# Optimization experiments

Measured on AMD Instinct MI355X. Metric: run time of the kernel, lower is better.

The kernel has to match this reference:

```python
import jax, jax.numpy as jnp
import numpy as np

N_NODES = 50000
N_EDGES = 800000
D_IN = 16


def gcn_conv(x, edge_index, W, b, n_nodes):
    """PyG GCNConv: x' = D^{-1/2} (A + I) D^{-1/2} X W + b (add_self_loops=True)."""
    h = x @ W  # [N, d_out] - transform before propagate (small d => cheaper)
    src = jnp.concatenate([edge_index[0], jnp.arange(n_nodes)])  # add self-loops
    dst = jnp.concatenate([edge_index[1], jnp.arange(n_nodes)])
    deg = jax.ops.segment_sum(jnp.ones_like(dst, dtype=h.dtype), dst,
                              num_segments=n_nodes)  # in-degree incl. self-loop
    deg_inv_sqrt = jnp.where(deg > 0, jax.lax.rsqrt(deg), 0.0)
    norm = deg_inv_sqrt[src] * deg_inv_sqrt[dst]  # [E+N]
    msg = h[src] * norm[:, None]                  # gather + scale
    out = jax.ops.segment_sum(msg, dst, num_segments=n_nodes)  # scatter-add
    return out + b


def setup_inputs() -> dict:
    key = jax.random.key(0)
    ks = jax.random.split(key, 16)
    d = D_IN
    x = jax.random.normal(ks[0], (N_NODES, d), dtype=jnp.float32)
    edge_index = jax.random.randint(ks[1], (2, N_EDGES), 0, N_NODES, dtype=jnp.int64)

    def glorot(k, fan_in, fan_out):
        s = (6.0 / (fan_in + fan_out)) ** 0.5
        return jax.random.uniform(k, (fan_in, fan_out), jnp.float32, -s, s)

    return {
        "x": x,
        "edge_index": edge_index,
        "W1": glorot(ks[2], d, 2 * d),      "b1": jnp.zeros((2 * d,), jnp.float32),
        "W2": glorot(ks[3], 2 * d, 4 * d),  "b2": jnp.zeros((4 * d,), jnp.float32),
        "W3": glorot(ks[4], 4 * d, 8 * d),  "b3": jnp.zeros((8 * d,), jnp.float32),
        "Wl1": glorot(ks[5], 8 * d, 4 * d), "bl1": jnp.zeros((4 * d,), jnp.float32),
        "Wl2": glorot(ks[6], 4 * d, 2 * d), "bl2": jnp.zeros((2 * d,), jnp.float32),
        "Wl3": glorot(ks[7], 2 * d, d),     "bl3": jnp.zeros((d,), jnp.float32),
    }


def reference(x, edge_index, W1, b1, W2, b2, W3, b3, Wl1, bl1, Wl2, bl2, Wl3, bl3):
    n = x.shape[0]
    # note: original applies relu twice per conv; relu is idempotent
    out = jax.nn.relu(gcn_conv(x, edge_index, W1, b1, n))
    out = jax.nn.relu(gcn_conv(out, edge_index, W2, b2, n))
    out = jax.nn.relu(gcn_conv(out, edge_index, W3, b3, n))
    out = jax.nn.relu(out @ Wl1 + bl1)
    out = jax.nn.relu(out @ Wl2 + bl2)
    out = jax.nn.relu(out @ Wl3 + bl3)
    return out
```

## Files before the change

### kernel.cpp

```cpp
#include <hip/hip_runtime.h>

#define TPB 256
#define TE  2048
#define MAXB 6144

typedef _Float16 half_t;
typedef _Float16 half4 __attribute__((ext_vector_type(4)));
typedef _Float16 half8 __attribute__((ext_vector_type(8)));
typedef float float8v __attribute__((ext_vector_type(8)));

static inline int cdiv(int a, int b) { return (a + b - 1) / b; }


__global__ void k_zero_int(int* p, int n) {
    int i = blockIdx.x * blockDim.x + threadIdx.x;
    if (i < n) p[i] = 0;
}

__global__ void k_bhist(const int* __restrict__ dst, int* __restrict__ gcnt,
                        int e, int nb) {
    __shared__ int lc[256];
    for (int t = threadIdx.x; t < nb; t += TPB) lc[t] = 0;
    __syncthreads();
    for (int i = blockIdx.x * TPB + threadIdx.x; i < e; i += gridDim.x * TPB)
        atomicAdd(&lc[dst[i] >> 8], 1);
    __syncthreads();
    for (int t = threadIdx.x; t < nb; t += TPB) {
        int v = lc[t];
        if (v) atomicAdd(&gcnt[t], v);
    }
}

__global__ void __launch_bounds__(TPB)
k_binscatter(const int* __restrict__ src, const int* __restrict__ dst,
             const int* __restrict__ gcnt, int* __restrict__ bcur2,
             unsigned int* __restrict__ gbuf, int e, int nb) {
    __shared__ int lcnt[256], loffs[256], lcur[256], gres[256];
    __shared__ int ss[256];
    __shared__ unsigned int ldata[TE];
    const int tid = threadIdx.x;
    const int base = blockIdx.x * TE;
    const int cnt = min(TE, e - base);

    {
        int v = (tid < nb) ? gcnt[tid] : 0;
        ss[tid] = v;
        __syncthreads();
        for (int d = 1; d < 256; d <<= 1) {
            int x2 = (tid >= d) ? ss[tid - d] : 0;
            __syncthreads();
            ss[tid] += x2;
            __syncthreads();
        }
        gres[tid] = ss[tid] - v;
        lcnt[tid] = 0;
    }
    __syncthreads();

    unsigned int myv[TE / TPB];
    int myb[TE / TPB];
#pragma unroll
    for (int k = 0; k < TE / TPB; ++k) {
        int j = tid + k * TPB;
        if (j < cnt) {
            int d = dst[base + j], s = src[base + j];
            int b = d >> 8;
            myv[k] = ((unsigned)b << 24) | ((unsigned)(d & 255) << 16) | (unsigned)s;
            myb[k] = b;
            atomicAdd(&lcnt[b], 1);
        } else myb[k] = -1;
    }
    __syncthreads();
    {
        int v = (tid < nb) ? lcnt[tid] : 0;
        ss[tid] = v;
        __syncthreads();
        for (int d = 1; d < 256; d <<= 1) {
            int x2 = (tid >= d) ? ss[tid - d] : 0;
            __syncthreads();
            ss[tid] += x2;
            __syncthreads();
        }
        if (tid < nb) { loffs[tid] = ss[tid] - v; lcur[tid] = ss[tid] - v; }
    }
    __syncthreads();
    if (tid < nb && lcnt[tid]) gres[tid] += atomicAdd(&bcur2[tid], lcnt[tid]);
#pragma unroll
    for (int k = 0; k < TE / TPB; ++k) {
        if (myb[k] >= 0) {
            int p = atomicAdd(&lcur[myb[k]], 1);
            ldata[p] = myv[k];
        }
    }
    __syncthreads();
    for (int j = tid; j < cnt; j += TPB) {
        unsigned int v = ldata[j];
        int b = v >> 24;
        gbuf[gres[b] + (j - loffs[b])] = v & 0xFFFFFFu;
    }
}

__global__ void __launch_bounds__(TPB)
k_csr(const unsigned int* __restrict__ gbuf, const int* __restrict__ gcnt,
      const float* __restrict__ x, int* __restrict__ offs,
      float* __restrict__ dinv, unsigned short* __restrict__ ssrc,
      half_t* __restrict__ G, int n, int e, int nb) {
    __shared__ int ss[256], cnt[256], loffs2[256], lcur2[256];
    __shared__ float sdinv[256];
    __shared__ unsigned short stage[MAXB];
    const int b = blockIdx.x;
    const int t = threadIdx.x;

    {
        int v = (t < nb) ? gcnt[t] : 0;
        ss[t] = v;
        __syncthreads();
        for (int d = 1; d < 256; d <<= 1) {
            int x2 = (t >= d) ? ss[t - d] : 0;
            __syncthreads();
            ss[t] += x2;
            __syncthreads();
        }
    }
    const int s0 = (b > 0) ? ss[b - 1] : 0;
    const int s1 = ss[b];
    const int m = s1 - s0;
    __syncthreads();
    cnt[t] = 0;
    __syncthreads();
    for (int j = t; j < m; j += TPB)
        atomicAdd(&cnt[(gbuf[s0 + j] >> 16) & 255], 1);
    __syncthreads();
    {
        int v = cnt[t];
        ss[t] = v;
        __syncthreads();
        for (int d = 1; d < 256; d <<= 1) {
            int x2 = (t >= d) ? ss[t - d] : 0;
            __syncthreads();
            ss[t] += x2;
            __syncthreads();
        }
        loffs2[t] = ss[t] - v;
        lcur2[t] = ss[t] - v;
        float di = rsqrtf((float)v + 1.0f);
        sdinv[t] = di;
        int node = b * 256 + t;
        if (node < n) {
            offs[node] = s0 + loffs2[t];
            dinv[node] = di;
        }
    }
    __syncthreads();
    for (int j = t; j < m; j += TPB) {
        unsigned int v = gbuf[s0 + j];
        int p = atomicAdd(&lcur2[(v >> 16) & 255], 1);
        stage[p] = (unsigned short)(v & 0xFFFFu);
    }
    __syncthreads();
    for (int j = t; j < m; j += TPB) ssrc[s0 + j] = stage[j];
    if (b == 0 && t == 0) offs[n] = e;

    const int base = b * 256;
    const int cn = min(256, n - base);
    const float4* X4 = (const float4*)x;
    half4* G4 = (half4*)G;
    for (int j = t; j < cn * 4; j += TPB) {
        int nl = j >> 2, k4 = j & 3;
        float4 v = X4[(size_t)(base + nl) * 4 + k4];
        float d = sdinv[nl];
        half4 h;
        h.x = (half_t)(v.x * d); h.y = (half_t)(v.y * d);
        h.z = (half_t)(v.z * d); h.w = (half_t)(v.w * d);
        G4[(size_t)(base + nl) * 4 + k4] = h;
    }
}

template<int DI, int DO, int R, bool SCALE, bool OUT_HALF, bool WHALF>
__global__ void __launch_bounds__(TPB, 4)
k_conv(const int* __restrict__ offs, const unsigned short* __restrict__ ssrc,
       const half_t* __restrict__ G, const float* __restrict__ dinv,
       const float* __restrict__ W, const float* __restrict__ b,
       void* __restrict__ outp, int n) {
    constexpr int CT = DO / 4;
    constexpr int RT = TPB / CT;
    constexpr int TM = RT * R;
    constexpr int K4 = DI / 4;
    constexpr int PX = K4 + 1;
    constexpr int C  = DI / 8;
    static_assert(TM * C == TPB, "gather/gemm tile mismatch");
    __shared__ float4 sW4[WHALF ? 1 : DI * CT];
    __shared__ half4  sWh[WHALF ? DI * CT : 1];
    __shared__ float4 sX4[TM * PX];
    __shared__ int soffs[TM + 1];
    __shared__ unsigned char perm[TM];
    const int tid = threadIdx.x;
    const int r0 = blockIdx.x * TM;

    const float4* Wg = (const float4*)W;
    for (int t = tid; t < DI * CT; t += TPB) {
        float4 w = Wg[t];
        if (WHALF) {
            half4 h;
            h.x = (half_t)w.x; h.y = (half_t)w.y;
            h.z = (half_t)w.z; h.w = (half_t)w.w;
            sWh[t] = h;
        } else {
            sW4[t] = w;
        }
    }
    if (tid <= TM) soffs[tid] = offs[min(r0 + tid, n)];
    __syncthreads();
    if (tid < TM) {
        int d = soffs[tid + 1] - soffs[tid];
        int rank = 0;
        for (int j = 0; j < TM; ++j) {
            int dj = soffs[j + 1] - soffs[j];
            rank += (dj > d) || (dj == d && j < tid);
        }
        perm[rank] = (unsigned char)tid;
    }
    __syncthreads();

    {
        int slot = tid / C;
        int gc = tid - slot * C;
        int lrow = perm[slot];
        int row = r0 + lrow;
        float8v acc;
#pragma unroll
        for (int q = 0; q < 8; ++q) acc[q] = 0.f;
        if (row < n) {
            const half8* Grow = (const half8*)G;
            half8 hs = Grow[(size_t)row * C + gc];
#pragma unroll
            for (int q = 0; q < 8; ++q) acc[q] = (float)hs[q];
            int s0 = soffs[lrow], s1 = soffs[lrow + 1];
            int j = s0;
            for (; j + 3 < s1; j += 4) {
                int sa = ssrc[j], sb = ssrc[j + 1];
                int sc = ssrc[j + 2], sd = ssrc[j + 3];
                half8 ga = Grow[(size_t)sa * C + gc];
                half8 gb = Grow[(size_t)sb * C + gc];
                half8 gch = Grow[(size_t)sc * C + gc];
                half8 gd = Grow[(size_t)sd * C + gc];
#pragma unroll
                for (int q = 0; q < 8; ++q)
                    acc[q] += ((float)ga[q] + (float)gb[q]) + ((float)gch[q] + (float)gd[q]);
            }
            for (; j < s1; ++j) {
                half8 ga = Grow[(size_t)ssrc[j] * C + gc];
#pragma unroll
                for (int q = 0; q < 8; ++q) acc[q] += (float)ga[q];
            }
            float di = dinv[row];
#pragma unroll
            for (int q = 0; q < 8; ++q) acc[q] *= di;
        }
        sX4[lrow * PX + 2 * gc]     = make_float4(acc[0], acc[1], acc[2], acc[3]);
        sX4[lrow * PX + 2 * gc + 1] = make_float4(acc[4], acc[5], acc[6], acc[7]);
    }
    __syncthreads();

    const int c = tid & (CT - 1);
    const int rg = tid / CT;
    const int rbase = rg * R;
    float4 acc[R];
#pragma unroll
    for (int r = 0; r < R; ++r) acc[r] = make_float4(0.f, 0.f, 0.f, 0.f);

#pragma unroll 2
    for (int k4 = 0; k4 < K4; ++k4) {
        float4 xv[R];
#pragma unroll
        for (int r = 0; r < R; ++r) xv[r] = sX4[(rbase + r) * PX + k4];
#pragma unroll
        for (int kk = 0; kk < 4; ++kk) {
            float4 wv;
            if (WHALF) {
                half4 wh = sWh[(k4 * 4 + kk) * CT + c];
                wv = make_float4((float)wh.x, (float)wh.y, (float)wh.z, (float)wh.w);
            } else {
                wv = sW4[(k4 * 4 + kk) * CT + c];
            }
#pragma unroll
            for (int r = 0; r < R; ++r) {
                float xs = (kk == 0) ? xv[r].x : (kk == 1) ? xv[r].y
                         : (kk == 2) ? xv[r].z : xv[r].w;
                acc[r].x += xs * wv.x; acc[r].y += xs * wv.y;
                acc[r].z += xs * wv.z; acc[r].w += xs * wv.w;
            }
        }
    }

    float4 bc = ((const float4*)b)[c];
#pragma unroll
    for (int r = 0; r < R; ++r) {
        int row = r0 + rbase + r;
        if (row < n) {
            float4 o;
            o.x = fmaxf(acc[r].x + bc.x, 0.f);
            o.y = fmaxf(acc[r].y + bc.y, 0.f);
            o.z = fmaxf(acc[r].z + bc.z, 0.f);
            o.w = fmaxf(acc[r].w + bc.w, 0.f);
            if (SCALE) {
                float d = dinv[row];
                o.x *= d; o.y *= d; o.z *= d; o.w *= d;
            }
            if (OUT_HALF) {
                half4 h;
                h.x = (half_t)o.x; h.y = (half_t)o.y;
                h.z = (half_t)o.z; h.w = (half_t)o.w;
                ((half4*)outp)[(size_t)row * CT + c] = h;
            } else {
                ((float4*)outp)[(size_t)row * CT + c] = o;
            }
        }
    }
}

__global__ void __launch_bounds__(256, 2)
k_head(const half_t* __restrict__ X,
       const float* __restrict__ W1, const float* __restrict__ b1,
       const float* __restrict__ W2, const float* __restrict__ b2,
       const float* __restrict__ W3, const float* __restrict__ b3,
       float* __restrict__ out, int n) {
    __shared__ half_t hW1[128 * 64];
    __shared__ half_t hW2[64 * 32];
    __shared__ half_t hW3[32 * 16];
    __shared__ float h1[64 * 65];
    __shared__ float h2[64 * 33];
    const int tid = threadIdx.x;
    const int r0 = blockIdx.x * 64;

    for (int t = tid; t < 128 * 64; t += 256) hW1[t] = (half_t)W1[t];
    for (int t = tid; t < 64 * 32; t += 256) hW2[t] = (half_t)W2[t];
    for (int t = tid; t < 32 * 16; t += 256) hW3[t] = (half_t)W3[t];
    __syncthreads();

    {
        const int c4 = tid & 15;
        const int rowg = tid >> 4;
        const half8* Xr = (const half8*)X;
        float acc[4][4];
#pragma unroll
        for (int r = 0; r < 4; ++r)
#pragma unroll
            for (int j = 0; j < 4; ++j) acc[r][j] = 0.f;
        for (int k8 = 0; k8 < 16; ++k8) {
            half8 xh[4];
#pragma unroll
            for (int r = 0; r < 4; ++r) {
                int row = r0 + rowg * 4 + r;
                if (row < n) xh[r] = Xr[(size_t)row * 16 + k8];
                else { half8 z; for (int q = 0; q < 8; ++q) z[q] = (half_t)0.f; xh[r] = z; }
            }
#pragma unroll
            for (int q = 0; q < 8; ++q) {
                int k = k8 * 8 + q;
                half4 w = *(const half4*)&hW1[k * 64 + c4 * 4];
                float w0 = (float)w.x, w1 = (float)w.y, w2 = (float)w.z, w3 = (float)w.w;
#pragma unroll
                for (int r = 0; r < 4; ++r) {
                    float xs = (float)xh[r][q];
                    acc[r][0] += xs * w0; acc[r][1] += xs * w1;
                    acc[r][2] += xs * w2; acc[r][3] += xs * w3;
                }
            }
        }
        float4 bc = ((const float4*)b1)[c4];
#pragma unroll
        for (int r = 0; r < 4; ++r) {
            int rl = rowg * 4 + r;
            h1[rl * 65 + c4 * 4 + 0] = fmaxf(acc[r][0] + bc.x, 0.f);
            h1[rl * 65 + c4 * 4 + 1] = fmaxf(acc[r][1] + bc.y, 0.f);
            h1[rl * 65 + c4 * 4 + 2] = fmaxf(acc[r][2] + bc.z, 0.f);
            h1[rl * 65 + c4 * 4 + 3] = fmaxf(acc[r][3] + bc.w, 0.f);
        }
    }
    __syncthreads();

    {
        const int c4 = tid & 7;
        const int rowg = tid >> 3;
        float acc[2][4];
#pragma unroll
        for (int r = 0; r < 2; ++r)
#pragma unroll
            for (int j = 0; j < 4; ++j) acc[r][j] = 0.f;
#pragma unroll 4
        for (int k = 0; k < 64; ++k) {
            half4 w = *(const half4*)&hW2[k * 32 + c4 * 4];
            float w0 = (float)w.x, w1 = (float)w.y, w2 = (float)w.z, w3 = (float)w.w;
#pragma unroll
            for (int r = 0; r < 2; ++r) {
                float xs = h1[(rowg * 2 + r) * 65 + k];
                acc[r][0] += xs * w0; acc[r][1] += xs * w1;
                acc[r][2] += xs * w2; acc[r][3] += xs * w3;
            }
        }
        float4 bc = ((const float4*)b2)[c4];
#pragma unroll
        for (int r = 0; r < 2; ++r) {
            int rl = rowg * 2 + r;
            h2[rl * 33 + c4 * 4 + 0] = fmaxf(acc[r][0] + bc.x, 0.f);
            h2[rl * 33 + c4 * 4 + 1] = fmaxf(acc[r][1] + bc.y, 0.f);
            h2[rl * 33 + c4 * 4 + 2] = fmaxf(acc[r][2] + bc.z, 0.f);
            h2[rl * 33 + c4 * 4 + 3] = fmaxf(acc[r][3] + bc.w, 0.f);
        }
    }
    __syncthreads();

    {
        const int c4 = tid & 3;
        const int rl = tid >> 2;
        float a0 = 0.f, a1 = 0.f, a2 = 0.f, a3 = 0.f;
#pragma unroll 4
        for (int k = 0; k < 32; ++k) {
            half4 w = *(const half4*)&hW3[k * 16 + c4 * 4];
            float xs = h2[rl * 33 + k];
            a0 += xs * (float)w.x; a1 += xs * (float)w.y;
            a2 += xs * (float)w.z; a3 += xs * (float)w.w;
        }
        int row = r0 + rl;
        if (row < n) {
            float4 bc = ((const float4*)b3)[c4];
            float4 o;
            o.x = fmaxf(a0 + bc.x, 0.f);
            o.y = fmaxf(a1 + bc.y, 0.f);
            o.z = fmaxf(a2 + bc.z, 0.f);
            o.w = fmaxf(a3 + bc.w, 0.f);
            ((float4*)out)[(size_t)row * 4 + c4] = o;
        }
    }
}

extern "C" void kernel_launch(void* const* d_in, const int* in_sizes, int n_in,
                              void* d_out, int out_size, void* d_ws, size_t ws_size,
                              hipStream_t stream) {
    const float* x   = (const float*)d_in[0];
    const int*   ei  = (const int*)d_in[1];
    const float* W1  = (const float*)d_in[2];
    const float* bb1 = (const float*)d_in[3];
    const float* W2  = (const float*)d_in[4];
    const float* bb2 = (const float*)d_in[5];
    const float* W3  = (const float*)d_in[6];
    const float* bb3 = (const float*)d_in[7];
    const float* Wl1 = (const float*)d_in[8];
    const float* bl1 = (const float*)d_in[9];
    const float* Wl2 = (const float*)d_in[10];
    const float* bl2 = (const float*)d_in[11];
    const float* Wl3 = (const float*)d_in[12];
    const float* bl3 = (const float*)d_in[13];
    float* out = (float*)d_out;

    const int n = in_sizes[0] / 16;
    const int e = in_sizes[1] / 2;
    const int* src = ei;
    const int* dst = ei + e;
    const int nb = cdiv(n, 256);

    char* p = (char*)d_ws;
    auto alloc = [&](size_t bytes) {
        char* r = p;
        p += (bytes + 255) & ~(size_t)255;
        return r;
    };
    float*          dinv   = (float*)         alloc((size_t)n * 4);
    int*            offs   = (int*)           alloc((size_t)(n + 1) * 4);
    int*            gcnt   = (int*)           alloc(256 * 4);
    int*            bcur2  = (int*)           alloc(256 * 4);
    unsigned int*   gbuf   = (unsigned int*)  alloc((size_t)e * 4);
    unsigned short* ssrc   = (unsigned short*)alloc((size_t)e * 2);
    half_t*         H1     = (half_t*)        alloc((size_t)n * 64 * 2);
    half_t*         H2     = (half_t*)        alloc((size_t)n * 32 * 2);
    half_t*         X3h    = (half_t*)        alloc((size_t)n * 128 * 2);

    k_zero_int<<<2, 256, 0, stream>>>(gcnt, 512);
    k_bhist<<<512, TPB, 0, stream>>>(dst, gcnt, e, nb);
    k_binscatter<<<cdiv(e, TE), TPB, 0, stream>>>(src, dst, gcnt, bcur2, gbuf, e, nb);
    k_csr<<<nb, TPB, 0, stream>>>(gbuf, gcnt, x, offs, dinv, ssrc, H1, n, e, nb);

    k_conv<16, 32, 4, true, true, false><<<cdiv(n, 128), TPB, 0, stream>>>(
        offs, ssrc, H1, dinv, W1, bb1, H2, n);
    k_conv<32, 64, 4, true, true, false><<<cdiv(n, 64), TPB, 0, stream>>>(
        offs, ssrc, H2, dinv, W2, bb2, H1, n);
    k_conv<64, 128, 4, false, true, true><<<cdiv(n, 32), TPB, 0, stream>>>(
        offs, ssrc, H1, dinv, W3, bb3, X3h, n);

    k_head<<<cdiv(n, 64), 256, 0, stream>>>(X3h, Wl1, bl1, Wl2, bl2, Wl3, bl3, out, n);
}
```

Before: 222.0 us.

## Use packed fp16 dot2 instructions for conv and head GEMMs, drop degree sort

Replaces the fp32 FMA inner products in the conv GEMM (when FDOT is set) and in the first head layer with v_dot2 fp16 instructions. Weights are repacked into a k-contiguous half8 layout and gathered activations are staged in shared memory as fp16. It also removes the per-block degree-ranking permutation used to balance gather work across threads. This cuts ALU work and shared-memory footprint, at the cost of lower precision in the activations and possible gather load imbalance.

```diff
diff --git a/kernel.cpp b/kernel.cpp
--- a/kernel.cpp
+++ b/kernel.cpp
@@ -5,11 +5,27 @@
 #define MAXB 6144
 
 typedef _Float16 half_t;
+typedef _Float16 half2_t __attribute__((ext_vector_type(2)));
 typedef _Float16 half4 __attribute__((ext_vector_type(4)));
 typedef _Float16 half8 __attribute__((ext_vector_type(8)));
 typedef float float8v __attribute__((ext_vector_type(8)));
 
 static inline int cdiv(int a, int b) { return (a + b - 1) / b; }
+
+__device__ __forceinline__ float dot8(half8 a, half8 b, float acc) {
+#if __has_builtin(__builtin_amdgcn_fdot2)
+    acc = __builtin_amdgcn_fdot2(half2_t{a[0], a[1]}, half2_t{b[0], b[1]}, acc, false);
+    acc = __builtin_amdgcn_fdot2(half2_t{a[2], a[3]}, half2_t{b[2], b[3]}, acc, false);
+    acc = __builtin_amdgcn_fdot2(half2_t{a[4], a[5]}, half2_t{b[4], b[5]}, acc, false);
+    acc = __builtin_amdgcn_fdot2(half2_t{a[6], a[7]}, half2_t{b[6], b[7]}, acc, false);
+#else
+#pragma unroll
+    for (int q = 0; q < 8; ++q) acc += (float)a[q] * (float)b[q];
+#endif
+    return acc;
+}
+
+#define WPACK(k, cg, CT) (((((k) >> 3) * 4 + ((cg) & 3)) * (CT) + ((cg) >> 2)) * 8 + ((k) & 7))
 
 
 __global__ void k_zero_int(int* p, int n) {
@@ -176,7 +192,7 @@
     }
 }
 
-template<int DI, int DO, int R, bool SCALE, bool OUT_HALF, bool WHALF>
+template<int DI, int DO, int R, bool SCALE, bool OUT_HALF, bool FDOT>
 __global__ void __launch_bounds__(TPB, 4)
 k_conv(const int* __restrict__ offs, const unsigned short* __restrict__ ssrc,
        const half_t* __restrict__ G, const float* __restrict__ dinv,
@@ -186,46 +202,34 @@
     constexpr int RT = TPB / CT;
     constexpr int TM = RT * R;
     constexpr int K4 = DI / 4;
+    constexpr int K8 = DI / 8;
     constexpr int PX = K4 + 1;
+    constexpr int XP = DI + 8;
     constexpr int C  = DI / 8;
     static_assert(TM * C == TPB, "gather/gemm tile mismatch");
-    __shared__ float4 sW4[WHALF ? 1 : DI * CT];
-    __shared__ half4  sWh[WHALF ? DI * CT : 1];
-    __shared__ float4 sX4[TM * PX];
+    __shared__ __align__(16) float4 sW4[FDOT ? 1 : DI * CT];
+    __shared__ __align__(16) half_t sWp[FDOT ? DI * DO : 8];
+    __shared__ __align__(16) float4 sX4[FDOT ? 1 : TM * PX];
+    __shared__ __align__(16) half_t sXh[FDOT ? TM * XP : 8];
     __shared__ int soffs[TM + 1];
-    __shared__ unsigned char perm[TM];
     const int tid = threadIdx.x;
     const int r0 = blockIdx.x * TM;
 
-    const float4* Wg = (const float4*)W;
-    for (int t = tid; t < DI * CT; t += TPB) {
-        float4 w = Wg[t];
-        if (WHALF) {
-            half4 h;
-            h.x = (half_t)w.x; h.y = (half_t)w.y;
-            h.z = (half_t)w.z; h.w = (half_t)w.w;
-            sWh[t] = h;
-        } else {
-            sW4[t] = w;
-        }
+    if (FDOT) {
+        for (int t = tid; t < DI * DO; t += TPB) {
+            int k = t / DO, cg = t - k * DO;
+            sWp[WPACK(k, cg, CT)] = (half_t)W[t];
+        }
+    } else {
+        const float4* Wg = (const float4*)W;
+        for (int t = tid; t < DI * CT; t += TPB) sW4[t] = Wg[t];
     }
     if (tid <= TM) soffs[tid] = offs[min(r0 + tid, n)];
     __syncthreads();
-    if (tid < TM) {
-        int d = soffs[tid + 1] - soffs[tid];
-        int rank = 0;
-        for (int j = 0; j < TM; ++j) {
-            int dj = soffs[j + 1] - soffs[j];
-            rank += (dj > d) || (dj == d && j < tid);
-        }
-        perm[rank] = (unsigned char)tid;
-    }
-    __syncthreads();
-
-    {
-        int slot = tid / C;
-        int gc = tid - slot * C;
-        int lrow = perm[slot];
+
+    {
+        int lrow = tid / C;
+        int gc = tid - lrow * C;
         int row = r0 + lrow;
         float8v acc;
 #pragma unroll
@@ -257,38 +261,60 @@
 #pragma unroll
             for (int q = 0; q < 8; ++q) acc[q] *= di;
         }
-        sX4[lrow * PX + 2 * gc]     = make_float4(acc[0], acc[1], acc[2], acc[3]);
-        sX4[lrow * PX + 2 * gc + 1] = make_float4(acc[4], acc[5], acc[6], acc[7]);
+        if (FDOT) {
+            half8 h;
+#pragma unroll
+            for (int q = 0; q < 8; ++q) h[q] = (half_t)acc[q];
+            *(half8*)&sXh[lrow * XP + gc * 8] = h;
+        } else {
+            sX4[lrow * PX + 2 * gc]     = make_float4(acc[0], acc[1], acc[2], acc[3]);
+            sX4[lrow * PX + 2 * gc + 1] = make_float4(acc[4], acc[5], acc[6], acc[7]);
+        }
     }
     __syncthreads();
 
     const int c = tid & (CT - 1);
     const int rg = tid / CT;
     const int rbase = rg * R;
-    float4 acc[R];
-#pragma unroll
-    for (int r = 0; r < R; ++r) acc[r] = make_float4(0.f, 0.f, 0.f, 0.f);
-
+    float accf[R][4];
+#pragma unroll
+    for (int r = 0; r < R; ++r)
+#pragma unroll
+        for (int j = 0; j < 4; ++j) accf[r][j] = 0.f;
+
+    if (FDOT) {
+#pragma unroll
+        for (int k8 = 0; k8 < K8; ++k8) {
+            half8 xh[R];
+#pragma unroll
+            for (int r = 0; r < R; ++r)
+                xh[r] = *(const half8*)&sXh[(rbase + r) * XP + k8 * 8];
+            half8 wv[4];
+#pragma unroll
+            for (int j = 0; j < 4; ++j)
+                wv[j] = *(const half8*)&sWp[(((k8 * 4 + j) * CT) + c) * 8];
+#pragma unroll
+            for (int j = 0; j < 4; ++j)
+#pragma unroll
+                for (int r = 0; r < R; ++r)
+                    accf[r][j] = dot8(xh[r], wv[j], accf[r][j]);
+        }
+    } else {
 #pragma unroll 2
-    for (int k4 = 0; k4 < K4; ++k4) {
-        float4 xv[R];
-#pragma unroll
-        for (int r = 0; r < R; ++r) xv[r] = sX4[(rbase + r) * PX + k4];
-#pragma unroll
-        for (int kk = 0; kk < 4; ++kk) {
-            float4 wv;
-            if (WHALF) {
-                half4 wh = sWh[(k4 * 4 + kk) * CT + c];
-                wv = make_float4((float)wh.x, (float)wh.y, (float)wh.z, (float)wh.w);
-            } else {
-                wv = sW4[(k4 * 4 + kk) * CT + c];
-            }
-#pragma unroll
-            for (int r = 0; r < R; ++r) {
-                float xs = (kk == 0) ? xv[r].x : (kk == 1) ? xv[r].y
-                         : (kk == 2) ? xv[r].z : xv[r].w;
-                acc[r].x += xs * wv.x; acc[r].y += xs * wv.y;
-                acc[r].z += xs * wv.z; acc[r].w += xs * wv.w;
+        for (int k4 = 0; k4 < K4; ++k4) {
+            float4 xv[R];
+#pragma unroll
+            for (int r = 0; r < R; ++r) xv[r] = sX4[(rbase + r) * PX + k4];
+#pragma unroll
+            for (int kk = 0; kk < 4; ++kk) {
+                float4 wv = sW4[(k4 * 4 + kk) * CT + c];
+#pragma unroll
+                for (int r = 0; r < R; ++r) {
+                    float xs = (kk == 0) ? xv[r].x : (kk == 1) ? xv[r].y
+                             : (kk == 2) ? xv[r].z : xv[r].w;
+                    accf[r][0] += xs * wv.x; accf[r][1] += xs * wv.y;
+                    accf[r][2] += xs * wv.z; accf[r][3] += xs * wv.w;
+                }
             }
         }
     }
@@ -299,10 +325,10 @@
         int row = r0 + rbase + r;
         if (row < n) {
             float4 o;
-            o.x = fmaxf(acc[r].x + bc.x, 0.f);
-            o.y = fmaxf(acc[r].y + bc.y, 0.f);
-            o.z = fmaxf(acc[r].z + bc.z, 0.f);
-            o.w = fmaxf(acc[r].w + bc.w, 0.f);
+            o.x = fmaxf(accf[r][0] + bc.x, 0.f);
+            o.y = fmaxf(accf[r][1] + bc.y, 0.f);
+            o.z = fmaxf(accf[r][2] + bc.z, 0.f);
+            o.w = fmaxf(accf[r][3] + bc.w, 0.f);
             if (SCALE) {
                 float d = dinv[row];
                 o.x *= d; o.y *= d; o.z *= d; o.w *= d;
@@ -325,7 +351,7 @@
        const float* __restrict__ W2, const float* __restrict__ b2,
        const float* __restrict__ W3, const float* __restrict__ b3,
        float* __restrict__ out, int n) {
-    __shared__ half_t hW1[128 * 64];
+    __shared__ __align__(16) half_t hW1p[128 * 64];
     __shared__ half_t hW2[64 * 32];
     __shared__ half_t hW3[32 * 16];
     __shared__ float h1[64 * 65];
@@ -333,7 +359,10 @@
     const int tid = threadIdx.x;
     const int r0 = blockIdx.x * 64;
 
-    for (int t = tid; t < 128 * 64; t += 256) hW1[t] = (half_t)W1[t];
+    for (int t = tid; t < 128 * 64; t += 256) {
+        int k = t >> 6, cg = t & 63;
+        hW1p[WPACK(k, cg, 16)] = (half_t)W1[t];
+    }
     for (int t = tid; t < 64 * 32; t += 256) hW2[t] = (half_t)W2[t];
     for (int t = tid; t < 32 * 16; t += 256) hW3[t] = (half_t)W3[t];
     __syncthreads();
@@ -347,6 +376,7 @@
         for (int r = 0; r < 4; ++r)
 #pragma unroll
             for (int j = 0; j < 4; ++j) acc[r][j] = 0.f;
+#pragma unroll 4
         for (int k8 = 0; k8 < 16; ++k8) {
             half8 xh[4];
 #pragma unroll
@@ -355,18 +385,15 @@
                 if (row < n) xh[r] = Xr[(size_t)row * 16 + k8];
                 else { half8 z; for (int q = 0; q < 8; ++q) z[q] = (half_t)0.f; xh[r] = z; }
             }
-#pragma unroll
-            for (int q = 0; q < 8; ++q) {
-                int k = k8 * 8 + q;
-                half4 w = *(const half4*)&hW1[k * 64 + c4 * 4];
-                float w0 = (float)w.x, w1 = (float)w.y, w2 = (float)w.z, w3 = (float)w.w;
-#pragma unroll
-                for (int r = 0; r < 4; ++r) {
-                    float xs = (float)xh[r][q];
-                    acc[r][0] += xs * w0; acc[r][1] += xs * w1;
-                    acc[r][2] += xs * w2; acc[r][3] += xs * w3;
-                }
-            }
+            half8 wv[4];
+#pragma unroll
+            for (int j = 0; j < 4; ++j)
+                wv[j] = *(const half8*)&hW1p[(((k8 * 4 + j) * 16) + c4) * 8];
+#pragma unroll
+            for (int j = 0; j < 4; ++j)
+#pragma unroll
+                for (int r = 0; r < 4; ++r)
+                    acc[r][j] = dot8(xh[r], wv[j], acc[r][j]);
         }
         float4 bc = ((const float4*)b1)[c4];
 #pragma unroll
```

Measured after the change: 319.0 us. 43.7% more time.
